# Kernel optimization log

Measured on AMD Instinct MI355X. Metric: run time of the kernel, lower is better.

The kernel has to match this reference:

```python
import jax, jax.numpy as jnp
import numpy as np

CHANNELS_CHOICE = np.array([8, 16, 24, 32, 40, 48, 56, 64])
MAX_C = 64
B, H, W_SP = 128, 32, 32
N_EDGES = 6
# edge list per intermediate node: (edge_weight_index, source_node_index)
EDGES = [[(0, 0)], [(1, 0), (2, 1)], [(3, 0), (4, 1), (5, 2)]]


def setup_inputs() -> dict:
    key = jax.random.key(0)
    k1, k2, k3, k4 = jax.random.split(key, 4)
    inputs = jax.random.normal(k1, (B, MAX_C, H, W_SP), dtype=jnp.float32)
    alphas1 = jax.random.uniform(k2, (8,), dtype=jnp.float32)  # input-width arch weights
    alphas2 = jax.random.uniform(k3, (8,), dtype=jnp.float32)  # output-width arch weights
    # shared master 3x3 conv weight per edge (OIHW)
    W = jax.random.normal(k4, (N_EDGES, MAX_C, MAX_C, 3, 3), dtype=jnp.float32) * 0.05
    return {"inputs": inputs, "alphas1": alphas1, "alphas2": alphas2, "W": W}


def _channel_scale(alphas1, alphas2, dtype):
    # mask[c, i] = 1 if channel c is inside width choice CHANNELS_CHOICE[i]
    mask = (jnp.arange(MAX_C)[:, None] < jnp.asarray(CHANNELS_CHOICE)[None, :]).astype(dtype)  # [64, 8]
    a_in = mask @ alphas1   # [64] cumulative input-channel weight
    a_out = mask @ alphas2  # [64] cumulative output-channel weight
    return a_out[:, None] * a_in[None, :]  # [64, 64]


def _edge(x, w, scale):
    # weighted-combi of all (c1, c2) channel-sliced sub-convs == one conv with scaled weight
    w_eff = w * scale[:, :, None, None]
    return jax.lax.conv_general_dilated(
        jax.nn.relu(x), w_eff, window_strides=(1, 1), padding="SAME",
        dimension_numbers=("NCHW", "OIHW", "NCHW"))


def reference(inputs, alphas1, alphas2, W):
    scale = _channel_scale(alphas1, alphas2, inputs.dtype)
    nodes = [inputs]
    for node_edges in EDGES:
        feat = 0.0
        for l, src in node_edges:
            feat = feat + _edge(nodes[src], W[l], scale)
        nodes.append(feat)
    return nodes[-1]
```

## Files before the change

### kernel.cpp

```cpp
#include <hip/hip_runtime.h>
#include <hip/hip_bf16.h>


typedef __bf16 bf16x8 __attribute__((ext_vector_type(8)));
typedef float floatx4 __attribute__((ext_vector_type(4)));
typedef unsigned int uint32;

#define PADW 34
#define PIMG (PADW * PADW)
#define ROWB (PADW * 64 * 2)
#define A_LDS (10 * ROWB)
#define TAPB (64 * 64 * 2)
#define A_CHUNKS (A_LDS / 16)

__device__ __forceinline__ void gld16(const char* g, char* l) {
    __builtin_amdgcn_global_load_lds(
        (const __attribute__((address_space(1))) uint32*)g,
        (__attribute__((address_space(3))) uint32*)l, 16, 0, 0);
}

__global__ void prep_weights(const float* __restrict__ a1,
                             const float* __restrict__ a2,
                             const float* __restrict__ W,
                             __hip_bfloat16* __restrict__ wt) {
    int idx = blockIdx.x * 256 + threadIdx.x;
    int i = idx & 63;
    int o = (idx >> 6) & 63;
    int rest = idx >> 12;
    int t = rest % 9;
    int l = rest / 9;
    int ji = i >> 3, jo = o >> 3;
    float ain = 0.f, aout = 0.f;
#pragma unroll
    for (int j = 0; j < 8; ++j) {
        ain  += (j >= ji) ? a1[j] : 0.f;
        aout += (j >= jo) ? a2[j] : 0.f;
    }
    float v = W[(size_t)((l * 64 + o) * 64 + i) * 9 + t] * ain * aout;
    size_t e = (size_t)(l * 9 + t) * 4096 + o * 64 +
               ((((i >> 3) ^ (o & 7)) << 3) + (i & 7));
    wt[e] = __float2bfloat16(v);
}

__global__ void relu_pad(const float* __restrict__ in,
                         __hip_bfloat16* __restrict__ r0) {
    __shared__ float tile[32][65];
    int b = blockIdx.x >> 5, y = blockIdx.x & 31;
    int tid = threadIdx.x;
    int x = tid & 31, c0 = tid >> 5;
    const float* ip = in + ((size_t)b * 64 * 32 + y) * 32 + x;
#pragma unroll
    for (int cc = 0; cc < 8; ++cc) {
        int c = cc * 8 + c0;
        tile[x][c] = fmaxf(ip[(size_t)c * 1024], 0.f);
    }
    __syncthreads();
    int o = tid & 63, xg = tid >> 6;
    int p0 = (b * PADW + y + 1) * PADW + 1;
#pragma unroll
    for (int xx = 0; xx < 8; ++xx) {
        int xq = xx * 4 + xg;
        int p = p0 + xq;
        size_t e = (size_t)p * 64 + ((((o >> 3) ^ (p & 7)) << 3) + (o & 7));
        r0[e] = __float2bfloat16(tile[xq][o]);
    }
}

__global__ void zero_halo(__hip_bfloat16* r0, __hip_bfloat16* r1,
                          __hip_bfloat16* r2) {
    int b = blockIdx.x;
    int tid = threadIdx.x;
    __hip_bfloat16* bufs[3] = {r0, r1, r2};
#pragma unroll
    for (int f = 0; f < 3; ++f) {
        uint32* buf = (uint32*)(bufs[f] + (size_t)b * PIMG * 64);
        for (int idx = tid; idx < 132 * 32; idx += 256) {
            int slot = idx >> 5, u = idx & 31;
            int yy, xx;
            if (slot < 34)      { yy = 0;  xx = slot; }
            else if (slot < 68) { yy = 33; xx = slot - 34; }
            else { int s2 = slot - 68; yy = 1 + (s2 >> 1); xx = (s2 & 1) * 33; }
            buf[(size_t)(yy * PADW + xx) * 32 + u] = 0u;
        }
    }
}

template <int NSRC, bool FINAL>
__global__ __launch_bounds__(256) void conv_stage(
    const __hip_bfloat16* __restrict__ s0,
    const __hip_bfloat16* __restrict__ s1,
    const __hip_bfloat16* __restrict__ s2,
    const __hip_bfloat16* __restrict__ wt,
    void* __restrict__ dstv, int l0) {
    __shared__ char smem[A_LDS + 2 * TAPB];
    int tid = threadIdx.x;
    int wv = tid >> 6, lane = tid & 63;
    int quad = lane >> 4, l15 = lane & 15;
    int blk = blockIdx.x;
    int b = blk >> 2, y0 = (blk & 3) << 3;

    const char* srcs[3] = {(const char*)s0, (const char*)s1, (const char*)s2};
    const char* gW = (const char*)wt + (size_t)l0 * 9 * (size_t)TAPB;

    auto stage_A = [&](int s) {
        const char* gA = srcs[s] + (size_t)(b * PADW + y0) * PADW * 128;
#pragma unroll
        for (int it = 0; it < 11; ++it) {
            int c = it * 256 + tid;
            if (it < 10 || tid < 160)
                gld16(gA + (size_t)c * 16, smem + (it * 256 + wv * 64) * 16);
        }
    };
    auto stage_B = [&](int T) {
        const char* gB = gW + (size_t)T * TAPB;
        char* dst = smem + A_LDS + (T & 1) * TAPB;
#pragma unroll
        for (int it = 0; it < 2; ++it)
            gld16(gB + (size_t)(it * 256 + tid) * 16,
                  dst + (it * 256 + wv * 64) * 16);
    };

    floatx4 acc[4][4];
#pragma unroll
    for (int m = 0; m < 4; ++m)
#pragma unroll
        for (int n = 0; n < 4; ++n) acc[m][n] = (floatx4){0.f, 0.f, 0.f, 0.f};

    stage_A(0);
    stage_B(0);
    __syncthreads();

#pragma unroll
    for (int T = 0; T < 9 * NSRC; ++T) {
        int s = T / 9, tl = T % 9, ky = tl / 3, kx = tl % 3, buf = T & 1;
        if (T + 1 < 9 * NSRC) stage_B(T + 1);

#pragma unroll
        for (int q = 0; q < 2; ++q) {
            bf16x8 Af[4], Bf[4];
#pragma unroll
            for (int m = 0; m < 4; ++m) {
                int arow = 2 * wv + (m >> 1) + ky;
                int apx  = ((m & 1) << 4) + l15 + kx;
                int R = b * PADW + y0 + arow;
                int slot = ((q << 2) + quad) ^ ((2 * R + apx) & 7);
                Af[m] = *(const bf16x8*)(smem + arow * ROWB +
                                         apx * 128 + slot * 16);
            }
#pragma unroll
            for (int n = 0; n < 4; ++n) {
                int o = (n << 4) + l15;
                int slot = ((q << 2) + quad) ^ (l15 & 7);
                Bf[n] = *(const bf16x8*)(smem + A_LDS + buf * TAPB +
                                         o * 128 + slot * 16);
            }
#pragma unroll
            for (int m = 0; m < 4; ++m)
#pragma unroll
                for (int n = 0; n < 4; ++n)
                    acc[m][n] = __builtin_amdgcn_mfma_f32_16x16x32_bf16(
                        Af[m], Bf[n], acc[m][n], 0, 0, 0);
        }

        if (T + 1 < 9 * NSRC) {
            __syncthreads();
            if (tl == 8) {
                stage_A(s + 1);
                __syncthreads();
            }
        }
    }

    if (FINAL) {
        float* out = (float*)dstv;
#pragma unroll
        for (int m = 0; m < 4; ++m) {
            int row = y0 + 2 * wv + (m >> 1);
#pragma unroll
            for (int n = 0; n < 4; ++n) {
                int o = (n << 4) + l15;
#pragma unroll
                for (int r = 0; r < 4; ++r) {
                    int x = ((m & 1) << 4) + (quad << 2) + r;
                    out[(((size_t)b * 64 + o) * 32 + row) * 32 + x] = acc[m][n][r];
                }
            }
        }
    } else {
        __hip_bfloat16* out = (__hip_bfloat16*)dstv;
#pragma unroll
        for (int m = 0; m < 4; ++m) {
            int row = y0 + 2 * wv + (m >> 1);
#pragma unroll
            for (int n = 0; n < 4; ++n) {
                int o = (n << 4) + l15;
#pragma unroll
                for (int r = 0; r < 4; ++r) {
                    int x = ((m & 1) << 4) + (quad << 2) + r;
                    int p = (b * PADW + row + 1) * PADW + x + 1;
                    float v = fmaxf(acc[m][n][r], 0.f);
                    size_t e = (size_t)p * 64 +
                               ((((o >> 3) ^ (p & 7)) << 3) + (o & 7));
                    out[e] = __float2bfloat16(v);
                }
            }
        }
    }
}

extern "C" void kernel_launch(void* const* d_in, const int* in_sizes, int n_in,
                              void* d_out, int out_size, void* d_ws,
                              size_t ws_size, hipStream_t stream) {
    const float* inputs  = (const float*)d_in[0];
    const float* alphas1 = (const float*)d_in[1];
    const float* alphas2 = (const float*)d_in[2];
    const float* W       = (const float*)d_in[3];
    char* ws = (char*)d_ws;

    __hip_bfloat16* wt = (__hip_bfloat16*)(ws);
    __hip_bfloat16* r0 = (__hip_bfloat16*)(ws + ((size_t)1 << 20));
    __hip_bfloat16* r1 = (__hip_bfloat16*)(ws + ((size_t)20 << 20));
    __hip_bfloat16* r2 = (__hip_bfloat16*)(ws + ((size_t)40 << 20));
    float* out = (float*)d_out;

    prep_weights<<<864, 256, 0, stream>>>(alphas1, alphas2, W, wt);
    relu_pad<<<128 * 32, 256, 0, stream>>>(inputs, r0);
    zero_halo<<<128, 256, 0, stream>>>(r0, r1, r2);

    conv_stage<1, false><<<512, 256, 0, stream>>>(r0, r1, r2, wt, (void*)r1, 0);
    conv_stage<2, false><<<512, 256, 0, stream>>>(r0, r1, r2, wt, (void*)r2, 1);
    conv_stage<3, true ><<<512, 256, 0, stream>>>(r0, r1, r2, wt, (void*)out, 3);
}
```

Baseline: 159.8 us.

## Load conv weights directly to registers, drop per-tap barriers, fuse prep kernels

Weight fragments are now loaded straight from global memory into registers with a one-tap prefetch, instead of being double-buffered through LDS. This removes the per-tap block barrier and the swizzled weight layout. The three preprocessing kernels are merged into one launch, and the final fp32 output is written with vector stores. In exchange, weight traffic now comes from L2 for every wave and register pressure rises.

```diff
diff --git a/kernel.cpp b/kernel.cpp
--- a/kernel.cpp
+++ b/kernel.cpp
@@ -10,8 +10,8 @@
 #define PIMG (PADW * PADW)
 #define ROWB (PADW * 64 * 2)
 #define A_LDS (10 * ROWB)
+#define A_PAD (11 * 256 * 16)
 #define TAPB (64 * 64 * 2)
-#define A_CHUNKS (A_LDS / 16)
 
 __device__ __forceinline__ void gld16(const char* g, char* l) {
     __builtin_amdgcn_global_load_lds(
@@ -19,68 +19,65 @@
         (__attribute__((address_space(3))) uint32*)l, 16, 0, 0);
 }
 
-__global__ void prep_weights(const float* __restrict__ a1,
-                             const float* __restrict__ a2,
-                             const float* __restrict__ W,
-                             __hip_bfloat16* __restrict__ wt) {
-    int idx = blockIdx.x * 256 + threadIdx.x;
-    int i = idx & 63;
-    int o = (idx >> 6) & 63;
-    int rest = idx >> 12;
-    int t = rest % 9;
-    int l = rest / 9;
-    int ji = i >> 3, jo = o >> 3;
-    float ain = 0.f, aout = 0.f;
-#pragma unroll
-    for (int j = 0; j < 8; ++j) {
-        ain  += (j >= ji) ? a1[j] : 0.f;
-        aout += (j >= jo) ? a2[j] : 0.f;
-    }
-    float v = W[(size_t)((l * 64 + o) * 64 + i) * 9 + t] * ain * aout;
-    size_t e = (size_t)(l * 9 + t) * 4096 + o * 64 +
-               ((((i >> 3) ^ (o & 7)) << 3) + (i & 7));
-    wt[e] = __float2bfloat16(v);
-}
-
-__global__ void relu_pad(const float* __restrict__ in,
-                         __hip_bfloat16* __restrict__ r0) {
+__global__ __launch_bounds__(256) void pre_kernel(
+    const float* __restrict__ in, const float* __restrict__ a1,
+    const float* __restrict__ a2, const float* __restrict__ W,
+    __hip_bfloat16* __restrict__ wt, __hip_bfloat16* __restrict__ r0,
+    __hip_bfloat16* __restrict__ r1, __hip_bfloat16* __restrict__ r2) {
     __shared__ float tile[32][65];
-    int b = blockIdx.x >> 5, y = blockIdx.x & 31;
+    int blk = blockIdx.x;
     int tid = threadIdx.x;
-    int x = tid & 31, c0 = tid >> 5;
-    const float* ip = in + ((size_t)b * 64 * 32 + y) * 32 + x;
-#pragma unroll
-    for (int cc = 0; cc < 8; ++cc) {
-        int c = cc * 8 + c0;
-        tile[x][c] = fmaxf(ip[(size_t)c * 1024], 0.f);
-    }
-    __syncthreads();
-    int o = tid & 63, xg = tid >> 6;
-    int p0 = (b * PADW + y + 1) * PADW + 1;
-#pragma unroll
-    for (int xx = 0; xx < 8; ++xx) {
-        int xq = xx * 4 + xg;
-        int p = p0 + xq;
-        size_t e = (size_t)p * 64 + ((((o >> 3) ^ (p & 7)) << 3) + (o & 7));
-        r0[e] = __float2bfloat16(tile[xq][o]);
-    }
-}
-
-__global__ void zero_halo(__hip_bfloat16* r0, __hip_bfloat16* r1,
-                          __hip_bfloat16* r2) {
-    int b = blockIdx.x;
-    int tid = threadIdx.x;
-    __hip_bfloat16* bufs[3] = {r0, r1, r2};
-#pragma unroll
-    for (int f = 0; f < 3; ++f) {
-        uint32* buf = (uint32*)(bufs[f] + (size_t)b * PIMG * 64);
-        for (int idx = tid; idx < 132 * 32; idx += 256) {
-            int slot = idx >> 5, u = idx & 31;
-            int yy, xx;
-            if (slot < 34)      { yy = 0;  xx = slot; }
-            else if (slot < 68) { yy = 33; xx = slot - 34; }
-            else { int s2 = slot - 68; yy = 1 + (s2 >> 1); xx = (s2 & 1) * 33; }
-            buf[(size_t)(yy * PADW + xx) * 32 + u] = 0u;
+
+    if (blk < 864) {
+        int idx = blk * 256 + tid;
+        int i = idx & 63;
+        int o = (idx >> 6) & 63;
+        int rest = idx >> 12;
+        int t = rest % 9;
+        int l = rest / 9;
+        int ji = i >> 3, jo = o >> 3;
+        float ain = 0.f, aout = 0.f;
+#pragma unroll
+        for (int j = 0; j < 8; ++j) {
+            ain  += (j >= ji) ? a1[j] : 0.f;
+            aout += (j >= jo) ? a2[j] : 0.f;
+        }
+        float v = W[(size_t)((l * 64 + o) * 64 + i) * 9 + t] * ain * aout;
+        wt[(size_t)(l * 9 + t) * 4096 + o * 64 + i] = __float2bfloat16(v);
+    } else if (blk < 992) {
+        int b = blk - 864;
+        __hip_bfloat16* bufs[3] = {r0, r1, r2};
+#pragma unroll
+        for (int f = 0; f < 3; ++f) {
+            uint32* buf = (uint32*)(bufs[f] + (size_t)b * PIMG * 64);
+            for (int idx = tid; idx < 132 * 32; idx += 256) {
+                int slot = idx >> 5, u = idx & 31;
+                int yy, xx;
+                if (slot < 34)      { yy = 0;  xx = slot; }
+                else if (slot < 68) { yy = 33; xx = slot - 34; }
+                else { int s2 = slot - 68; yy = 1 + (s2 >> 1); xx = (s2 & 1) * 33; }
+                buf[(size_t)(yy * PADW + xx) * 32 + u] = 0u;
+            }
+        }
+    } else {
+        int rb = blk - 992;
+        int b = rb >> 5, y = rb & 31;
+        int x = tid & 31, c0 = tid >> 5;
+        const float* ip = in + ((size_t)b * 64 * 32 + y) * 32 + x;
+#pragma unroll
+        for (int cc = 0; cc < 8; ++cc) {
+            int c = cc * 8 + c0;
+            tile[x][c] = fmaxf(ip[(size_t)c * 1024], 0.f);
+        }
+        __syncthreads();
+        int o = tid & 63, xg = tid >> 6;
+        int p0 = (b * PADW + y + 1) * PADW + 1;
+#pragma unroll
+        for (int xx = 0; xx < 8; ++xx) {
+            int xq = xx * 4 + xg;
+            int p = p0 + xq;
+            size_t e = (size_t)p * 64 + ((((o >> 3) ^ (p & 7)) << 3) + (o & 7));
+            r0[e] = __float2bfloat16(tile[xq][o]);
         }
     }
 }
@@ -92,7 +89,7 @@
     const __hip_bfloat16* __restrict__ s2,
     const __hip_bfloat16* __restrict__ wt,
     void* __restrict__ dstv, int l0) {
-    __shared__ char smem[A_LDS + 2 * TAPB];
+    __shared__ char smem[A_PAD];
     int tid = threadIdx.x;
     int wv = tid >> 6, lane = tid & 63;
     int quad = lane >> 4, l15 = lane & 15;
@@ -100,24 +97,26 @@
     int b = blk >> 2, y0 = (blk & 3) << 3;
 
     const char* srcs[3] = {(const char*)s0, (const char*)s1, (const char*)s2};
-    const char* gW = (const char*)wt + (size_t)l0 * 9 * (size_t)TAPB;
+    const char* gB = (const char*)wt + (size_t)l0 * 9 * TAPB +
+                     l15 * 128 + quad * 16;
 
     auto stage_A = [&](int s) {
         const char* gA = srcs[s] + (size_t)(b * PADW + y0) * PADW * 128;
 #pragma unroll
-        for (int it = 0; it < 11; ++it) {
-            int c = it * 256 + tid;
-            if (it < 10 || tid < 160)
-                gld16(gA + (size_t)c * 16, smem + (it * 256 + wv * 64) * 16);
-        }
+        for (int it = 0; it < 11; ++it)
+            gld16(gA + (size_t)(it * 256 + tid) * 16,
+                  smem + (it * 256 + wv * 64) * 16);
     };
-    auto stage_B = [&](int T) {
-        const char* gB = gW + (size_t)T * TAPB;
-        char* dst = smem + A_LDS + (T & 1) * TAPB;
-#pragma unroll
-        for (int it = 0; it < 2; ++it)
-            gld16(gB + (size_t)(it * 256 + tid) * 16,
-                  dst + (it * 256 + wv * 64) * 16);
+
+    bf16x8 Bf[2][2][4];
+    auto load_B = [&](int T) {
+        const char* p = gB + (size_t)T * TAPB;
+#pragma unroll
+        for (int q = 0; q < 2; ++q)
+#pragma unroll
+            for (int n = 0; n < 4; ++n)
+                Bf[T & 1][q][n] =
+                    *(const bf16x8*)(p + n * 2048 + q * 64);
     };
 
     floatx4 acc[4][4];
@@ -127,17 +126,17 @@
         for (int n = 0; n < 4; ++n) acc[m][n] = (floatx4){0.f, 0.f, 0.f, 0.f};
 
     stage_A(0);
-    stage_B(0);
+    load_B(0);
     __syncthreads();
 
 #pragma unroll
     for (int T = 0; T < 9 * NSRC; ++T) {
-        int s = T / 9, tl = T % 9, ky = tl / 3, kx = tl % 3, buf = T & 1;
-        if (T + 1 < 9 * NSRC) stage_B(T + 1);
+        const int s = T / 9, tl = T % 9, ky = tl / 3, kx = tl % 3;
+        if (T + 1 < 9 * NSRC) load_B(T + 1);
 
 #pragma unroll
         for (int q = 0; q < 2; ++q) {
-            bf16x8 Af[4], Bf[4];
+            bf16x8 Af[4];
 #pragma unroll
             for (int m = 0; m < 4; ++m) {
                 int arow = 2 * wv + (m >> 1) + ky;
@@ -148,42 +147,30 @@
                                          apx * 128 + slot * 16);
             }
 #pragma unroll
+            for (int m = 0; m < 4; ++m)
+#pragma unroll
+                for (int n = 0; n < 4; ++n)
+                    acc[m][n] = __builtin_amdgcn_mfma_f32_16x16x32_bf16(
+                        Af[m], Bf[T & 1][q][n], acc[m][n], 0, 0, 0);
+        }
+
+        if (tl == 8 && s + 1 < NSRC) {
+            __syncthreads();
+            stage_A(s + 1);
+            __syncthreads();
+        }
+    }
+
+    if (FINAL) {
+        float* out = (float*)dstv;
+#pragma unroll
+        for (int m = 0; m < 4; ++m) {
+            int row = y0 + 2 * wv + (m >> 1);
+#pragma unroll
             for (int n = 0; n < 4; ++n) {
                 int o = (n << 4) + l15;
-                int slot = ((q << 2) + quad) ^ (l15 & 7);
-                Bf[n] = *(const bf16x8*)(smem + A_LDS + buf * TAPB +
-                                         o * 128 + slot * 16);
-            }
-#pragma unroll
-            for (int m = 0; m < 4; ++m)
-#pragma unroll
-                for (int n = 0; n < 4; ++n)
-                    acc[m][n] = __builtin_amdgcn_mfma_f32_16x16x32_bf16(
-                        Af[m], Bf[n], acc[m][n], 0, 0, 0);
-        }
-
-        if (T + 1 < 9 * NSRC) {
-            __syncthreads();
-            if (tl == 8) {
-                stage_A(s + 1);
-                __syncthreads();
-            }
-        }
-    }
-
-    if (FINAL) {
-        float* out = (float*)dstv;
-#pragma unroll
-        for (int m = 0; m < 4; ++m) {
-            int row = y0 + 2 * wv + (m >> 1);
-#pragma unroll
-            for (int n = 0; n < 4; ++n) {
-                int o = (n << 4) + l15;
-#pragma unroll
-                for (int r = 0; r < 4; ++r) {
-                    int x = ((m & 1) << 4) + (quad << 2) + r;
-                    out[(((size_t)b * 64 + o) * 32 + row) * 32 + x] = acc[m][n][r];
-                }
+                *(floatx4*)(out + (((size_t)b * 64 + o) * 32 + row) * 32 +
+                            ((m & 1) << 4) + (quad << 2)) = acc[m][n];
             }
         }
     } else {
@@ -223,10 +210,8 @@
     __hip_bfloat16* r2 = (__hip_bfloat16*)(ws + ((size_t)40 << 20));
     float* out = (float*)d_out;
 
-    prep_weights<<<864, 256, 0, stream>>>(alphas1, alphas2, W, wt);
-    relu_pad<<<128 * 32, 256, 0, stream>>>(inputs, r0);
-    zero_halo<<<128, 256, 0, stream>>>(r0, r1, r2);
-
+    pre_kernel<<<864 + 128 + 4096, 256, 0, stream>>>(inputs, alphas1, alphas2,
+                                                     W, wt, r0, r1, r2);
     conv_stage<1, false><<<512, 256, 0, stream>>>(r0, r1, r2, wt, (void*)r1, 0);
     conv_stage<2, false><<<512, 256, 0, stream>>>(r0, r1, r2, wt, (void*)r2, 1);
     conv_stage<3, true ><<<512, 256, 0, stream>>>(r0, r1, r2, wt, (void*)out, 3);
```

Measured after the change: 218.4 us. +36.7%, slower.
